# Kernel optimization log

Measured on AMD Instinct MI355X. Metric: run time of the kernel, lower is better.

The kernel has to match this reference:

```python
import jax, jax.numpy as jnp
import numpy as np

B, N, D = 8, 4096, 6          # clouds, points per cloud, coordinate dim
K = 64                        # max_num_neighbors in radius query
NS1, NS2 = 2048, 512          # fps ratios 0.5 and 0.25
R1, R2 = 0.2, 0.4             # ball-query radii
DIMS = {1: [6, 64, 64, 128], 2: [134, 128, 128, 256], 3: [262, 256, 512, 1024], 4: [1024, 512, 512]}


def setup_inputs():
    key = jax.random.key(0)
    k0, k1, k2 = jax.random.split(key, 3)
    inp = {}
    inp['synapse_cordi'] = jax.random.normal(k0, (B * N, D), jnp.float32)
    inp['batch_index'] = jnp.repeat(jnp.arange(B, dtype=jnp.int32), N)
    inp['weight'] = jax.random.uniform(k1, (B * N,), jnp.float32)
    k = k2
    for i, dims in DIMS.items():
        for j in range(len(dims) - 1):
            k, kw = jax.random.split(k)
            inp[f'w{i}_{j}'] = jax.random.normal(kw, (dims[j], dims[j + 1]), jnp.float32) * (1.0 / float(np.sqrt(dims[j])))
            inp[f'b{i}_{j}'] = jnp.zeros((dims[j + 1],), jnp.float32)
    return inp


def _mlp(x, params):
    # PyG MLP, plain_last=True; batch-norm at default (eval, running stats) is identity
    n = len(params)
    for i, (W, b) in enumerate(params):
        x = x @ W + b
        if i < n - 1:
            x = jax.nn.relu(x)
    return x


def _fps(pos, n_s):
    # farthest point sampling on one cloud [N, D] -> [n_s] indices (deterministic start at 0)
    d0 = jnp.sum((pos - pos[0]) ** 2, axis=-1)
    def step(mind, _):
        nxt = jnp.argmax(mind)
        mind = jnp.minimum(mind, jnp.sum((pos - pos[nxt]) ** 2, axis=-1))
        return mind, nxt
    _, idxs = jax.lax.scan(step, d0, None, length=n_s - 1)
    return jnp.concatenate([jnp.zeros((1,), idxs.dtype), idxs])


def _ball(pos, pos_q, r):
    # radius query: up to K nearest points within r for each query; [n_q,K] idx + validity mask
    d2 = jnp.sum((pos_q[:, None, :] - pos[None, :, :]) ** 2, axis=-1)  # [n_q, N]
    neg = jnp.where(d2 <= r * r, -d2, -jnp.inf)
    vals, nbr = jax.lax.top_k(neg, K)
    return nbr, vals > -jnp.inf


def _sa(x, pos, params, n_s, r):
    # Weight_Sample_Module: fps -> radius -> PointNetConv (gather, MLP, masked max-scatter)
    idx = jax.vmap(lambda p: _fps(p, n_s))(pos)                     # [B, n_s]
    pos_q = jnp.take_along_axis(pos, idx[..., None], axis=1)        # [B, n_s, D]
    nbr, valid = jax.vmap(lambda p, q: _ball(p, q, r))(pos, pos_q)  # [B, n_s, K]
    gather = lambda a: jax.vmap(lambda t, i: t[i])(a, nbr)          # [B, n_s, K, C]
    rel = gather(pos) - pos_q[:, :, None, :]
    feat = rel if x is None else jnp.concatenate([gather(x), rel], axis=-1)
    h = _mlp(feat, params)                                          # [B, n_s, K, C_out]
    h = jnp.where(valid[..., None], h, -jnp.inf)
    return jnp.max(h, axis=2), pos_q                                # max aggregation


def reference(synapse_cordi, batch_index, weight,
              w1_0, b1_0, w1_1, b1_1, w1_2, b1_2,
              w2_0, b2_0, w2_1, b2_1, w2_2, b2_2,
              w3_0, b3_0, w3_1, b3_1, w3_2, b3_2,
              w4_0, b4_0, w4_1, b4_1):
    pos = synapse_cordi.reshape(B, N, D)  # uniform clouds; batch_index = repeat(arange(B), N)
    p1 = [(w1_0, b1_0), (w1_1, b1_1), (w1_2, b1_2)]
    p2 = [(w2_0, b2_0), (w2_1, b2_1), (w2_2, b2_2)]
    p3 = [(w3_0, b3_0), (w3_1, b3_1), (w3_2, b3_2)]
    p4 = [(w4_0, b4_0), (w4_1, b4_1)]
    x1, pos1 = _sa(None, pos, p1, NS1, R1)   # [B, 2048, 128]
    x2, pos2 = _sa(x1, pos1, p2, NS2, R2)    # [B, 512, 256]
    h = _mlp(jnp.concatenate([x2, pos2], axis=-1), p3)  # [B, 512, 1024]
    g = jnp.max(h, axis=1)                   # global max pool -> [B, 1024]
    return _mlp(g, p4)                       # [B, 512]
```

## Files before the change

### kernel.cpp

```cpp
#include <hip/hip_runtime.h>
#include <math.h>

#define B_ 8
#define N_ 4096
#define D_ 6
#define K_ 64
#define NS1_ 2048
#define NS2_ 512

typedef float v2f __attribute__((ext_vector_type(2)));


__device__ __forceinline__ float dist2_rn(const float* __restrict__ a, const float* __restrict__ q) {
    float s = 0.f;
#pragma unroll
    for (int d = 0; d < 6; ++d) {
        float diff = __fsub_rn(a[d], q[d]);
        s = __fadd_rn(s, __fmul_rn(diff, diff));
    }
    return s;
}

__device__ __forceinline__ unsigned mapf(float x) {
    unsigned u = __float_as_uint(x);
    return (u & 0x80000000u) ? ~u : (u | 0x80000000u);
}
__device__ __forceinline__ float unmapf(unsigned u) {
    return __uint_as_float((u & 0x80000000u) ? (u & 0x7FFFFFFFu) : ~u);
}

template <int CTRL>
__device__ __forceinline__ double dppd(double k) {
    int lo = __double2loint(k), hi = __double2hiint(k);
    int nlo = __builtin_amdgcn_update_dpp(lo, lo, CTRL, 0xF, 0xF, false);
    int nhi = __builtin_amdgcn_update_dpp(hi, hi, CTRL, 0xF, 0xF, false);
    return __hiloint2double(nhi, nlo);
}


__device__ __forceinline__ void wait_flag(unsigned* f, int t) {
    if (t == 0) {
        while (__hip_atomic_load(f, __ATOMIC_RELAXED, __HIP_MEMORY_SCOPE_AGENT) == 0u)
            __builtin_amdgcn_s_sleep(32);
        __builtin_amdgcn_fence(__ATOMIC_ACQUIRE, "agent");
    }
    __syncthreads();
}


template <int NP, int NS>
__device__ __forceinline__ void fps_core(float* __restrict__ spos, int* __restrict__ sidx,
                                         double* __restrict__ part, int t) {
#pragma clang fp contract(off)
    constexpr int NT = 256;
    constexpr int P = NP / NT;
    constexpr int HP = P / 2;
    int lane = t & 63, w = t >> 6;

    v2f px2[HP][6];
#pragma unroll
    for (int j = 0; j < HP; ++j)
#pragma unroll
        for (int d = 0; d < 6; ++d) {
            px2[j][d].x = spos[(t + NT * (2 * j)) * 6 + d];
            px2[j][d].y = spos[(t + NT * (2 * j + 1)) * 6 + d];
        }

    float cx[6];
#pragma unroll
    for (int d = 0; d < 6; ++d) cx[d] = spos[d];

    v2f mind2[HP];
    float runv = -1.f;
    int runj = 0;
#pragma unroll
    for (int j = 0; j < HP; ++j) {
        v2f d2 = {0.f, 0.f};
#pragma unroll
        for (int d = 0; d < 6; ++d) {
            v2f df = px2[j][d] - cx[d];
            d2 = d2 + df * df;
        }
        mind2[j] = d2;
        if (d2.x > runv) { runv = d2.x; runj = t + NT * (2 * j); }
        if (d2.y > runv) { runv = d2.y; runj = t + NT * (2 * j + 1); }
    }

    for (int s = 1; s < NS; ++s) {
        double key = __hiloint2double((int)__float_as_uint(runv), (int)(unsigned)(~runj));
        key = fmax(key, dppd<0x111>(key));
        key = fmax(key, dppd<0x112>(key));
        key = fmax(key, dppd<0x114>(key));
        key = fmax(key, dppd<0x118>(key));
        key = fmax(key, dppd<0x142>(key));
        key = fmax(key, dppd<0x143>(key));
        if (lane == 63) part[(s & 1) * 4 + w] = key;
        __syncthreads();
        double kk = part[(s & 1) * 4 + (lane & 3)];
        kk = fmax(kk, dppd<0x111>(kk));
        kk = fmax(kk, dppd<0x112>(kk));
        int nx = ~__builtin_amdgcn_readlane(__double2loint(kk), 3);
        if (t == 0) sidx[s] = nx;

        const float2* sv2 = (const float2*)spos;
        float2 ca = sv2[nx * 3], cb = sv2[nx * 3 + 1], cc = sv2[nx * 3 + 2];
        cx[0] = ca.x; cx[1] = ca.y; cx[2] = cb.x; cx[3] = cb.y; cx[4] = cc.x; cx[5] = cc.y;

        runv = -1.f;
        runj = 0;
#pragma unroll
        for (int j = 0; j < HP; ++j) {
            v2f d2 = {0.f, 0.f};
#pragma unroll
            for (int d = 0; d < 6; ++d) {
                v2f df = px2[j][d] - cx[d];
                d2 = d2 + df * df;
            }
            float mx = fminf(mind2[j].x, d2.x);
            float my = fminf(mind2[j].y, d2.y);
            mind2[j].x = mx;
            mind2[j].y = my;
            if (mx > runv) { runv = mx; runj = t + NT * (2 * j); }
            if (my > runv) { runv = my; runj = t + NT * (2 * j + 1); }
        }
    }
}


template <int NPTS, int S>
__device__ __forceinline__ int ball_scan(const float* __restrict__ sp,
                                         const float* __restrict__ posq,
                                         float r2, int qid, int tid,
                                         float* __restrict__ sd, unsigned short* __restrict__ si) {
    float q[6];
#pragma unroll
    for (int d = 0; d < 6; ++d) q[d] = posq[(size_t)qid * 6 + d];

    int n = 0;
    float thr = INFINITY;
#pragma unroll 4
    for (int j = 0; j < NPTS; ++j) {
        float d2 = dist2_rn(sp + j * 6, q);
        if (d2 <= r2 && (n < K_ || d2 < thr)) {
            int i = (n < K_) ? n : (K_ - 1);
            if (n < K_) ++n;
            while (i > 0 && sd[(i - 1) * S + tid] > d2) {
                sd[i * S + tid] = sd[(i - 1) * S + tid];
                si[i * S + tid] = si[(i - 1) * S + tid];
                --i;
            }
            sd[i * S + tid] = d2;
            si[i * S + tid] = (unsigned short)j;
            if (n == K_) thr = sd[(K_ - 1) * S + tid];
        }
    }
    return n;
}


__global__ __launch_bounds__(256, 1) void stage12_kernel(
        const float* __restrict__ pos, float* __restrict__ pos1, float* __restrict__ pos2,
        float* __restrict__ x1, int* __restrict__ nbr2, int* __restrict__ cnt2,
        unsigned* __restrict__ g, unsigned* flags,
        const float* __restrict__ W1_0, const float* __restrict__ B1_0,
        const float* __restrict__ W1_1, const float* __restrict__ B1_1,
        const float* __restrict__ W1_2, const float* __restrict__ B1_2,
        float r2_1, float r2_2) {
    __shared__ union Smem {
        struct { float spos[N_ * 6]; int sidx[NS1_]; double part[8]; } fps;
        struct { float spos[N_ * 6]; float sd[K_ * 128]; unsigned short si[K_ * 128];
                 unsigned short scnt[128]; } p1;
        struct { float spos1[NS1_ * 6]; float sd2[K_ * 64]; unsigned short si2[K_ * 64]; } b2;
    } sm;
    int t = threadIdx.x;
    int lane = t & 63, w = t >> 6;

    if (blockIdx.x < 8) {
        int b = blockIdx.x;
        float* spos = sm.fps.spos;
        int* sidx = sm.fps.sidx;
        double* part = sm.fps.part;

        {
            const float4* src = (const float4*)(pos + (size_t)b * N_ * 6);
            float4* dst = (float4*)spos;
            for (int e = t; e < N_ * 6 / 4; e += 256) dst[e] = src[e];
        }
        if (t == 0) sidx[0] = 0;
        __syncthreads();

        fps_core<N_, NS1_>(spos, sidx, part, t);
        __syncthreads();

        float smp[NS1_ / 256][6];
#pragma unroll
        for (int i = 0; i < NS1_ / 256; ++i) {
            int s = t + 256 * i;
            int ix = sidx[s];
#pragma unroll
            for (int d = 0; d < 6; ++d) smp[i][d] = spos[ix * 6 + d];
        }
#pragma unroll
        for (int i = 0; i < NS1_ / 256; ++i) {
            int s = t + 256 * i;
#pragma unroll
            for (int d = 0; d < 6; ++d) pos1[((size_t)b * NS1_ + s) * 6 + d] = smp[i][d];
        }
        __syncthreads();
        if (t == 0) {
            __threadfence();
            __hip_atomic_store(&flags[b], 1u, __ATOMIC_RELEASE, __HIP_MEMORY_SCOPE_AGENT);
        }

#pragma unroll
        for (int i = 0; i < NS1_ / 256; ++i) {
            int s = t + 256 * i;
#pragma unroll
            for (int d = 0; d < 6; ++d) spos[s * 6 + d] = smp[i][d];
        }
        for (int e = t; e < 1024; e += 256) g[b * 1024 + e] = 0u;
        if (t == 0) sidx[0] = 0;
        __syncthreads();

        fps_core<NS1_, NS2_>(spos, sidx, part, t);
        __syncthreads();

        for (int s = t; s < NS2_; s += 256) {
            int ix = sidx[s];
#pragma unroll
            for (int d = 0; d < 6; ++d) pos2[((size_t)b * NS2_ + s) * 6 + d] = spos[ix * 6 + d];
        }
        __syncthreads();
        if (t == 0) {
            __threadfence();
            __hip_atomic_store(&flags[8 + b], 1u, __ATOMIC_RELEASE, __HIP_MEMORY_SCOPE_AGENT);
        }
    } else if (blockIdx.x < 8 + 128) {
        int blk = blockIdx.x - 8;
        int b = blk >> 4;
        {
            const float4* src = (const float4*)(pos + (size_t)b * N_ * 6);
            float4* dst = (float4*)sm.p1.spos;
            for (int e = t; e < N_ * 6 / 4; e += 256) dst[e] = src[e];
        }
        __syncthreads();
        wait_flag(&flags[b], t);

        int qbase1 = b * NS1_ + (blk & 15) * 128;
        if (t < 128) {
            int n = ball_scan<N_, 128>(sm.p1.spos, pos1, r2_1, qbase1 + t, t, sm.p1.sd, sm.p1.si);
            sm.p1.scnt[t] = (unsigned short)n;
        }
        __syncthreads();

        for (int qq = 0; qq < 32; ++qq) {
            int lq = w * 32 + qq;
            int qid = qbase1 + lq;
            float q[6];
#pragma unroll
            for (int d = 0; d < 6; ++d) q[d] = pos1[(size_t)qid * 6 + d];
            int c = sm.p1.scnt[lq];
            float m0 = -INFINITY, m1 = -INFINITY;
            for (int n = 0; n < c; ++n) {
                int j = sm.p1.si[n * 128 + lq];
                float rel[6];
#pragma unroll
                for (int d = 0; d < 6; ++d) rel[d] = sm.p1.spos[j * 6 + d] - q[d];
                float a = B1_0[lane];
#pragma unroll
                for (int d = 0; d < 6; ++d) a = fmaf(W1_0[d * 64 + lane], rel[d], a);
                float h1 = fmaxf(a, 0.f);
                float a2 = B1_1[lane];
                for (int k = 0; k < 64; ++k) {
                    float v = __shfl(h1, k, 64);
                    a2 = fmaf(W1_1[k * 64 + lane], v, a2);
                }
                float h2 = fmaxf(a2, 0.f);
                float o0 = B1_2[lane], o1 = B1_2[64 + lane];
                for (int k = 0; k < 64; ++k) {
                    float v = __shfl(h2, k, 64);
                    o0 = fmaf(W1_2[k * 128 + lane], v, o0);
                    o1 = fmaf(W1_2[k * 128 + 64 + lane], v, o1);
                }
                m0 = fmaxf(m0, o0);
                m1 = fmaxf(m1, o1);
            }
            x1[(size_t)qid * 128 + lane] = m0;
            x1[(size_t)qid * 128 + 64 + lane] = m1;
        }
    } else {
        int blk = blockIdx.x - 136;
        int b = blk >> 3;
        wait_flag(&flags[b], t);
        {
            const float4* src = (const float4*)(pos1 + (size_t)b * NS1_ * 6);
            float4* dst = (float4*)sm.b2.spos1;
            for (int e = t; e < NS1_ * 6 / 4; e += 256) dst[e] = src[e];
        }
        __syncthreads();
        wait_flag(&flags[8 + b], t);
        if (t < 64) {
            int qid = blk * 64 + t;
            int n = ball_scan<NS1_, 64>(sm.b2.spos1, pos2, r2_2, qid, t, sm.b2.sd2, sm.b2.si2);
            cnt2[qid] = n;
            for (int i = 0; i < n; ++i) nbr2[(size_t)qid * K_ + i] = (int)sm.b2.si2[i * 64 + t];
        }
    }
}


__global__ __launch_bounds__(256, 1) void sa2_mlp3_kernel(
        const float* __restrict__ pos1, const float* __restrict__ pos2,
        const int* __restrict__ nbr, const int* __restrict__ cnt,
        const float* __restrict__ x1,
        const float* __restrict__ W1, const float* __restrict__ B1,
        const float* __restrict__ W2, const float* __restrict__ B2,
        const float* __restrict__ W3, const float* __restrict__ B3,
        const float* __restrict__ M0, const float* __restrict__ MB0,
        const float* __restrict__ M1, const float* __restrict__ MB1,
        const float* __restrict__ M2, const float* __restrict__ MB2,
        unsigned* __restrict__ g) {
    __shared__ float sx2[16 * 256];
    int lane = threadIdx.x & 63;
    int w = threadIdx.x >> 6;
    int qbase = blockIdx.x * 16;
    int b = qbase >> 9;

    for (int qq = 0; qq < 4; ++qq) {
        int lq = w * 4 + qq;
        int qid = qbase + lq;
        float q[6];
#pragma unroll
        for (int d = 0; d < 6; ++d) q[d] = pos2[(size_t)qid * 6 + d];
        int c = cnt[qid];
        float m0 = -INFINITY, m1 = -INFINITY, m2 = -INFINITY, m3 = -INFINITY;
        for (int n = 0; n < c; ++n) {
            int j = nbr[(size_t)qid * K_ + n];
            size_t row = (size_t)b * NS1_ + j;
            const float* xs = x1 + row * 128;
            float rel[6];
#pragma unroll
            for (int d = 0; d < 6; ++d) rel[d] = pos1[row * 6 + d] - q[d];
            float a0e = B1[lane], a0o = 0.f, a1e = B1[64 + lane], a1o = 0.f;
            for (int k = 0; k < 128; k += 2) {
                float v0 = xs[k], v1 = xs[k + 1];
                a0e = fmaf(W1[k * 128 + lane], v0, a0e);
                a1e = fmaf(W1[k * 128 + 64 + lane], v0, a1e);
                a0o = fmaf(W1[(k + 1) * 128 + lane], v1, a0o);
                a1o = fmaf(W1[(k + 1) * 128 + 64 + lane], v1, a1o);
            }
            float a0 = a0e + a0o, a1 = a1e + a1o;
#pragma unroll
            for (int d = 0; d < 6; ++d) {
                float v = rel[d];
                a0 = fmaf(W1[(128 + d) * 128 + lane], v, a0);
                a1 = fmaf(W1[(128 + d) * 128 + 64 + lane], v, a1);
            }
            float h1a = fmaxf(a0, 0.f), h1b = fmaxf(a1, 0.f);
            float c0 = B2[lane], c1 = B2[64 + lane];
            for (int k = 0; k < 64; ++k) {
                float v = __shfl(h1a, k, 64);
                c0 = fmaf(W2[k * 128 + lane], v, c0);
                c1 = fmaf(W2[k * 128 + 64 + lane], v, c1);
            }
            for (int k = 0; k < 64; ++k) {
                float v = __shfl(h1b, k, 64);
                c0 = fmaf(W2[(64 + k) * 128 + lane], v, c0);
                c1 = fmaf(W2[(64 + k) * 128 + 64 + lane], v, c1);
            }
            float h2a = fmaxf(c0, 0.f), h2b = fmaxf(c1, 0.f);
            float e0 = B3[lane], e1 = B3[64 + lane], e2 = B3[128 + lane], e3 = B3[192 + lane];
            for (int k = 0; k < 64; ++k) {
                float v = __shfl(h2a, k, 64);
                e0 = fmaf(W3[k * 256 + lane], v, e0);
                e1 = fmaf(W3[k * 256 + 64 + lane], v, e1);
                e2 = fmaf(W3[k * 256 + 128 + lane], v, e2);
                e3 = fmaf(W3[k * 256 + 192 + lane], v, e3);
            }
            for (int k = 0; k < 64; ++k) {
                float v = __shfl(h2b, k, 64);
                e0 = fmaf(W3[(64 + k) * 256 + lane], v, e0);
                e1 = fmaf(W3[(64 + k) * 256 + 64 + lane], v, e1);
                e2 = fmaf(W3[(64 + k) * 256 + 128 + lane], v, e2);
                e3 = fmaf(W3[(64 + k) * 256 + 192 + lane], v, e3);
            }
            m0 = fmaxf(m0, e0);
            m1 = fmaxf(m1, e1);
            m2 = fmaxf(m2, e2);
            m3 = fmaxf(m3, e3);
        }
        sx2[lq * 256 + lane] = m0;
        sx2[lq * 256 + 64 + lane] = m1;
        sx2[lq * 256 + 128 + lane] = m2;
        sx2[lq * 256 + 192 + lane] = m3;
    }
    __syncthreads();

    int lq0 = w * 4;
    int qid0 = qbase + lq0;

    float xr[4][4];
#pragma unroll
    for (int q = 0; q < 4; ++q)
#pragma unroll
        for (int j = 0; j < 4; ++j) xr[q][j] = sx2[(lq0 + q) * 256 + j * 64 + lane];

    float a[4][4];
    {
        float4 bv = *(const float4*)&MB0[lane * 4];
#pragma unroll
        for (int q = 0; q < 4; ++q) { a[q][0] = bv.x; a[q][1] = bv.y; a[q][2] = bv.z; a[q][3] = bv.w; }
    }
#pragma unroll
    for (int j = 0; j < 4; ++j) {
        for (int k2 = 0; k2 < 64; ++k2) {
            int k = j * 64 + k2;
            float4 wv = *(const float4*)&M0[(size_t)k * 256 + lane * 4];
#pragma unroll
            for (int q = 0; q < 4; ++q) {
                float v = __shfl(xr[q][j], k2, 64);
                a[q][0] = fmaf(wv.x, v, a[q][0]);
                a[q][1] = fmaf(wv.y, v, a[q][1]);
                a[q][2] = fmaf(wv.z, v, a[q][2]);
                a[q][3] = fmaf(wv.w, v, a[q][3]);
            }
        }
    }
#pragma unroll
    for (int d = 0; d < 6; ++d) {
        float4 wv = *(const float4*)&M0[(size_t)(256 + d) * 256 + lane * 4];
#pragma unroll
        for (int q = 0; q < 4; ++q) {
            float v = pos2[(size_t)(qid0 + q) * 6 + d];
            a[q][0] = fmaf(wv.x, v, a[q][0]);
            a[q][1] = fmaf(wv.y, v, a[q][1]);
            a[q][2] = fmaf(wv.z, v, a[q][2]);
            a[q][3] = fmaf(wv.w, v, a[q][3]);
        }
    }
    float h1[4][4];
#pragma unroll
    for (int q = 0; q < 4; ++q)
#pragma unroll
        for (int u = 0; u < 4; ++u) h1[q][u] = fmaxf(a[q][u], 0.f);

    float c[4][8];
    {
        float4 b0 = *(const float4*)&MB1[lane * 8];
        float4 b1 = *(const float4*)&MB1[lane * 8 + 4];
#pragma unroll
        for (int q = 0; q < 4; ++q) {
            c[q][0] = b0.x; c[q][1] = b0.y; c[q][2] = b0.z; c[q][3] = b0.w;
            c[q][4] = b1.x; c[q][5] = b1.y; c[q][6] = b1.z; c[q][7] = b1.w;
        }
    }
    for (int l = 0; l < 64; ++l) {
#pragma unroll
        for (int r = 0; r < 4; ++r) {
            int k = l * 4 + r;
            float4 w0 = *(const float4*)&M1[(size_t)k * 512 + lane * 8];
            float4 w1 = *(const float4*)&M1[(size_t)k * 512 + lane * 8 + 4];
#pragma unroll
            for (int q = 0; q < 4; ++q) {
                float v = __shfl(h1[q][r], l, 64);
                c[q][0] = fmaf(w0.x, v, c[q][0]);
                c[q][1] = fmaf(w0.y, v, c[q][1]);
                c[q][2] = fmaf(w0.z, v, c[q][2]);
                c[q][3] = fmaf(w0.w, v, c[q][3]);
                c[q][4] = fmaf(w1.x, v, c[q][4]);
                c[q][5] = fmaf(w1.y, v, c[q][5]);
                c[q][6] = fmaf(w1.z, v, c[q][6]);
                c[q][7] = fmaf(w1.w, v, c[q][7]);
            }
        }
    }
    float h2[4][8];
#pragma unroll
    for (int q = 0; q < 4; ++q)
#pragma unroll
        for (int u = 0; u < 8; ++u) h2[q][u] = fmaxf(c[q][u], 0.f);

    float e[4][16];
#pragma unroll
    for (int jj = 0; jj < 4; ++jj) {
        float4 bv = *(const float4*)&MB2[lane * 16 + jj * 4];
#pragma unroll
        for (int q = 0; q < 4; ++q) {
            e[q][jj * 4 + 0] = bv.x; e[q][jj * 4 + 1] = bv.y;
            e[q][jj * 4 + 2] = bv.z; e[q][jj * 4 + 3] = bv.w;
        }
    }
    for (int l = 0; l < 64; ++l) {
#pragma unroll
        for (int r = 0; r < 8; ++r) {
            int k = l * 8 + r;
            const float* wp = &M2[(size_t)k * 1024 + lane * 16];
            float4 w0 = *(const float4*)&wp[0];
            float4 w1 = *(const float4*)&wp[4];
            float4 w2 = *(const float4*)&wp[8];
            float4 w3 = *(const float4*)&wp[12];
#pragma unroll
            for (int q = 0; q < 4; ++q) {
                float v = __shfl(h2[q][r], l, 64);
                e[q][0]  = fmaf(w0.x, v, e[q][0]);
                e[q][1]  = fmaf(w0.y, v, e[q][1]);
                e[q][2]  = fmaf(w0.z, v, e[q][2]);
                e[q][3]  = fmaf(w0.w, v, e[q][3]);
                e[q][4]  = fmaf(w1.x, v, e[q][4]);
                e[q][5]  = fmaf(w1.y, v, e[q][5]);
                e[q][6]  = fmaf(w1.z, v, e[q][6]);
                e[q][7]  = fmaf(w1.w, v, e[q][7]);
                e[q][8]  = fmaf(w2.x, v, e[q][8]);
                e[q][9]  = fmaf(w2.y, v, e[q][9]);
                e[q][10] = fmaf(w2.z, v, e[q][10]);
                e[q][11] = fmaf(w2.w, v, e[q][11]);
                e[q][12] = fmaf(w3.x, v, e[q][12]);
                e[q][13] = fmaf(w3.y, v, e[q][13]);
                e[q][14] = fmaf(w3.z, v, e[q][14]);
                e[q][15] = fmaf(w3.w, v, e[q][15]);
            }
        }
    }
#pragma unroll
    for (int u = 0; u < 16; ++u) {
        float m = fmaxf(fmaxf(e[0][u], e[1][u]), fmaxf(e[2][u], e[3][u]));
        atomicMax(&g[b * 1024 + lane * 16 + u], mapf(m));
    }
}


__global__ __launch_bounds__(512) void mlp4_kernel(const unsigned* __restrict__ g,
                                                   const float* __restrict__ W0, const float* __restrict__ B0,
                                                   const float* __restrict__ W1, const float* __restrict__ B1,
                                                   float* __restrict__ out) {
    int b = blockIdx.x;
    int c = threadIdx.x;
    __shared__ float h[512];
    float a0 = B0[c], a1 = 0.f, a2 = 0.f, a3 = 0.f;
    for (int k = 0; k < 1024; k += 4) {
        float v0 = unmapf(g[b * 1024 + k]);
        float v1 = unmapf(g[b * 1024 + k + 1]);
        float v2 = unmapf(g[b * 1024 + k + 2]);
        float v3 = unmapf(g[b * 1024 + k + 3]);
        a0 = fmaf(v0, W0[k * 512 + c], a0);
        a1 = fmaf(v1, W0[(k + 1) * 512 + c], a1);
        a2 = fmaf(v2, W0[(k + 2) * 512 + c], a2);
        a3 = fmaf(v3, W0[(k + 3) * 512 + c], a3);
    }
    h[c] = fmaxf((a0 + a1) + (a2 + a3), 0.f);
    __syncthreads();
    float o0 = B1[c], o1 = 0.f, o2 = 0.f, o3 = 0.f;
    for (int k = 0; k < 512; k += 4) {
        o0 = fmaf(h[k], W1[k * 512 + c], o0);
        o1 = fmaf(h[k + 1], W1[(k + 1) * 512 + c], o1);
        o2 = fmaf(h[k + 2], W1[(k + 2) * 512 + c], o2);
        o3 = fmaf(h[k + 3], W1[(k + 3) * 512 + c], o3);
    }
    out[(size_t)b * 512 + c] = (o0 + o1) + (o2 + o3);
}


extern "C" void kernel_launch(void* const* d_in, const int* in_sizes, int n_in,
                              void* d_out, int out_size, void* d_ws, size_t ws_size,
                              hipStream_t stream) {
    const float* pos = (const float*)d_in[0];
    const float* w1_0 = (const float*)d_in[3];
    const float* b1_0 = (const float*)d_in[4];
    const float* w1_1 = (const float*)d_in[5];
    const float* b1_1 = (const float*)d_in[6];
    const float* w1_2 = (const float*)d_in[7];
    const float* b1_2 = (const float*)d_in[8];
    const float* w2_0 = (const float*)d_in[9];
    const float* b2_0 = (const float*)d_in[10];
    const float* w2_1 = (const float*)d_in[11];
    const float* b2_1 = (const float*)d_in[12];
    const float* w2_2 = (const float*)d_in[13];
    const float* b2_2 = (const float*)d_in[14];
    const float* w3_0 = (const float*)d_in[15];
    const float* b3_0 = (const float*)d_in[16];
    const float* w3_1 = (const float*)d_in[17];
    const float* b3_1 = (const float*)d_in[18];
    const float* w3_2 = (const float*)d_in[19];
    const float* b3_2 = (const float*)d_in[20];
    const float* w4_0 = (const float*)d_in[21];
    const float* b4_0 = (const float*)d_in[22];
    const float* w4_1 = (const float*)d_in[23];
    const float* b4_1 = (const float*)d_in[24];
    float* out = (float*)d_out;

    char* ws = (char*)d_ws;
    size_t off = 0;
    float* pos1 = (float*)(ws + off);    off += (size_t)B_ * NS1_ * 6 * 4;
    float* pos2 = (float*)(ws + off);    off += (size_t)B_ * NS2_ * 6 * 4;
    float* x1 = (float*)(ws + off);      off += (size_t)B_ * NS1_ * 128 * 4;
    int* nbr2 = (int*)(ws + off);        off += (size_t)B_ * NS2_ * K_ * 4;
    int* cnt2 = (int*)(ws + off);        off += (size_t)B_ * NS2_ * 4;
    unsigned* g = (unsigned*)(ws + off); off += (size_t)B_ * 1024 * 4;
    unsigned* flags = (unsigned*)(ws + off); off += 16 * 4;

    const float r2_1 = (float)(0.2 * 0.2);
    const float r2_2 = (float)(0.4 * 0.4);

    hipMemsetAsync(flags, 0, 16 * 4, stream);

    stage12_kernel<<<200, 256, 0, stream>>>(pos, pos1, pos2, x1, nbr2, cnt2, g, flags,
                                            w1_0, b1_0, w1_1, b1_1, w1_2, b1_2,
                                            r2_1, r2_2);
    sa2_mlp3_kernel<<<(B_ * NS2_) / 16, 256, 0, stream>>>(pos1, pos2, nbr2, cnt2, x1,
                                                          w2_0, b2_0, w2_1, b2_1, w2_2, b2_2,
                                                          w3_0, b3_0, w3_1, b3_1, w3_2, b3_2, g);
    mlp4_kernel<<<B_, 512, 0, stream>>>(g, w4_0, b4_0, w4_1, b4_1, out);
}
```

Baseline: 2.498 ms.

## Fuse SA2, MLP3 and MLP4 into one persistent kernel with per-cloud flag counters

Merges the three launches into a single 200-block persistent kernel. The 128 SA1 blocks go on to run SA2 and MLP3 for their own cloud once counter flags report that SA1, FPS2 and ball-query results are ready. The FPS blocks finish with the final MLP4 once all 16 tail blocks for their cloud signal completion. Weights are pre-read into cache while blocks wait. This removes launch gaps and lets clouds proceed independently, but runs SA2/MLP3 on only 128 blocks instead of 256 and relies on all blocks being co-resident for the spin-waits.

After: 3.790 ms. +51.7%, slower.

```diff
diff --git a/kernel.cpp b/kernel.cpp
--- a/kernel.cpp
+++ b/kernel.cpp
@@ -45,6 +45,23 @@
         __builtin_amdgcn_fence(__ATOMIC_ACQUIRE, "agent");
     }
     __syncthreads();
+}
+
+__device__ __forceinline__ void wait_count(unsigned* f, unsigned tgt, int t) {
+    if (t == 0) {
+        while (__hip_atomic_load(f, __ATOMIC_RELAXED, __HIP_MEMORY_SCOPE_AGENT) < tgt)
+            __builtin_amdgcn_s_sleep(8);
+        __builtin_amdgcn_fence(__ATOMIC_ACQUIRE, "agent");
+    }
+    __syncthreads();
+}
+
+__device__ __forceinline__ void release_add(unsigned* f, int t) {
+    __syncthreads();
+    if (t == 0) {
+        __threadfence();
+        __hip_atomic_fetch_add(f, 1u, __ATOMIC_RELEASE, __HIP_MEMORY_SCOPE_AGENT);
+    }
 }
 
 
@@ -158,13 +175,275 @@
 }
 
 
-__global__ __launch_bounds__(256, 1) void stage12_kernel(
+__device__ __forceinline__ void sa2_one(int qid, int lane,
+        const float* __restrict__ pos1, const float* __restrict__ posq,
+        const int* __restrict__ nbr, const int* __restrict__ cnt,
+        const float* __restrict__ x1,
+        const float* __restrict__ W1, const float* __restrict__ B1,
+        const float* __restrict__ W2, const float* __restrict__ B2,
+        const float* __restrict__ W3, const float* __restrict__ B3,
+        float* __restrict__ out) {
+    int b = qid / NS2_;
+    float q[6];
+#pragma unroll
+    for (int d = 0; d < 6; ++d) q[d] = posq[(size_t)qid * 6 + d];
+    int c = cnt[qid];
+    float m0 = -INFINITY, m1 = -INFINITY, m2 = -INFINITY, m3 = -INFINITY;
+
+    for (int n = 0; n < c; ++n) {
+        int j = nbr[(size_t)qid * K_ + n];
+        size_t row = (size_t)b * NS1_ + j;
+        const float* xs = x1 + row * 128;
+        float rel[6];
+#pragma unroll
+        for (int d = 0; d < 6; ++d) rel[d] = pos1[row * 6 + d] - q[d];
+        float a0e = B1[lane], a0o = 0.f, a1e = B1[64 + lane], a1o = 0.f;
+        for (int k = 0; k < 128; k += 2) {
+            float v0 = xs[k], v1 = xs[k + 1];
+            a0e = fmaf(W1[k * 128 + lane], v0, a0e);
+            a1e = fmaf(W1[k * 128 + 64 + lane], v0, a1e);
+            a0o = fmaf(W1[(k + 1) * 128 + lane], v1, a0o);
+            a1o = fmaf(W1[(k + 1) * 128 + 64 + lane], v1, a1o);
+        }
+        float a0 = a0e + a0o, a1 = a1e + a1o;
+#pragma unroll
+        for (int d = 0; d < 6; ++d) {
+            float v = rel[d];
+            a0 = fmaf(W1[(128 + d) * 128 + lane], v, a0);
+            a1 = fmaf(W1[(128 + d) * 128 + 64 + lane], v, a1);
+        }
+        float h1a = fmaxf(a0, 0.f), h1b = fmaxf(a1, 0.f);
+        float c0 = B2[lane], c1 = B2[64 + lane];
+        for (int k = 0; k < 64; ++k) {
+            float v = __shfl(h1a, k, 64);
+            c0 = fmaf(W2[k * 128 + lane], v, c0);
+            c1 = fmaf(W2[k * 128 + 64 + lane], v, c1);
+        }
+        for (int k = 0; k < 64; ++k) {
+            float v = __shfl(h1b, k, 64);
+            c0 = fmaf(W2[(64 + k) * 128 + lane], v, c0);
+            c1 = fmaf(W2[(64 + k) * 128 + 64 + lane], v, c1);
+        }
+        float h2a = fmaxf(c0, 0.f), h2b = fmaxf(c1, 0.f);
+        float e0 = B3[lane], e1 = B3[64 + lane], e2 = B3[128 + lane], e3 = B3[192 + lane];
+        for (int k = 0; k < 64; ++k) {
+            float v = __shfl(h2a, k, 64);
+            e0 = fmaf(W3[k * 256 + lane], v, e0);
+            e1 = fmaf(W3[k * 256 + 64 + lane], v, e1);
+            e2 = fmaf(W3[k * 256 + 128 + lane], v, e2);
+            e3 = fmaf(W3[k * 256 + 192 + lane], v, e3);
+        }
+        for (int k = 0; k < 64; ++k) {
+            float v = __shfl(h2b, k, 64);
+            e0 = fmaf(W3[(64 + k) * 256 + lane], v, e0);
+            e1 = fmaf(W3[(64 + k) * 256 + 64 + lane], v, e1);
+            e2 = fmaf(W3[(64 + k) * 256 + 128 + lane], v, e2);
+            e3 = fmaf(W3[(64 + k) * 256 + 192 + lane], v, e3);
+        }
+        m0 = fmaxf(m0, e0);
+        m1 = fmaxf(m1, e1);
+        m2 = fmaxf(m2, e2);
+        m3 = fmaxf(m3, e3);
+    }
+    out[(size_t)qid * 256 + lane] = m0;
+    out[(size_t)qid * 256 + 64 + lane] = m1;
+    out[(size_t)qid * 256 + 128 + lane] = m2;
+    out[(size_t)qid * 256 + 192 + lane] = m3;
+}
+
+
+__device__ __forceinline__ void mlp3_wave(int qid0, int lane,
+        const float* __restrict__ x2, const float* __restrict__ pos2,
+        const float* __restrict__ M0, const float* __restrict__ MB0,
+        const float* __restrict__ M1, const float* __restrict__ MB1,
+        const float* __restrict__ M2, const float* __restrict__ MB2,
+        unsigned* __restrict__ g) {
+    int b = qid0 >> 9;
+
+    float xr[4][4];
+#pragma unroll
+    for (int q = 0; q < 4; ++q)
+#pragma unroll
+        for (int j = 0; j < 4; ++j) xr[q][j] = x2[(size_t)(qid0 + q) * 256 + j * 64 + lane];
+
+    float a[4][4];
+    {
+        float4 bv = *(const float4*)&MB0[lane * 4];
+#pragma unroll
+        for (int q = 0; q < 4; ++q) { a[q][0] = bv.x; a[q][1] = bv.y; a[q][2] = bv.z; a[q][3] = bv.w; }
+    }
+#pragma unroll
+    for (int j = 0; j < 4; ++j) {
+        for (int k2 = 0; k2 < 64; ++k2) {
+            int k = j * 64 + k2;
+            float4 wv = *(const float4*)&M0[(size_t)k * 256 + lane * 4];
+#pragma unroll
+            for (int q = 0; q < 4; ++q) {
+                float v = __shfl(xr[q][j], k2, 64);
+                a[q][0] = fmaf(wv.x, v, a[q][0]);
+                a[q][1] = fmaf(wv.y, v, a[q][1]);
+                a[q][2] = fmaf(wv.z, v, a[q][2]);
+                a[q][3] = fmaf(wv.w, v, a[q][3]);
+            }
+        }
+    }
+#pragma unroll
+    for (int d = 0; d < 6; ++d) {
+        float4 wv = *(const float4*)&M0[(size_t)(256 + d) * 256 + lane * 4];
+#pragma unroll
+        for (int q = 0; q < 4; ++q) {
+            float v = pos2[(size_t)(qid0 + q) * 6 + d];
+            a[q][0] = fmaf(wv.x, v, a[q][0]);
+            a[q][1] = fmaf(wv.y, v, a[q][1]);
+            a[q][2] = fmaf(wv.z, v, a[q][2]);
+            a[q][3] = fmaf(wv.w, v, a[q][3]);
+        }
+    }
+    float h1[4][4];
+#pragma unroll
+    for (int q = 0; q < 4; ++q)
+#pragma unroll
+        for (int u = 0; u < 4; ++u) h1[q][u] = fmaxf(a[q][u], 0.f);
+
+    float c[4][8];
+    {
+        float4 b0 = *(const float4*)&MB1[lane * 8];
+        float4 b1 = *(const float4*)&MB1[lane * 8 + 4];
+#pragma unroll
+        for (int q = 0; q < 4; ++q) {
+            c[q][0] = b0.x; c[q][1] = b0.y; c[q][2] = b0.z; c[q][3] = b0.w;
+            c[q][4] = b1.x; c[q][5] = b1.y; c[q][6] = b1.z; c[q][7] = b1.w;
+        }
+    }
+    for (int l = 0; l < 64; ++l) {
+#pragma unroll
+        for (int r = 0; r < 4; ++r) {
+            int k = l * 4 + r;
+            float4 w0 = *(const float4*)&M1[(size_t)k * 512 + lane * 8];
+            float4 w1 = *(const float4*)&M1[(size_t)k * 512 + lane * 8 + 4];
+#pragma unroll
+            for (int q = 0; q < 4; ++q) {
+                float v = __shfl(h1[q][r], l, 64);
+                c[q][0] = fmaf(w0.x, v, c[q][0]);
+                c[q][1] = fmaf(w0.y, v, c[q][1]);
+                c[q][2] = fmaf(w0.z, v, c[q][2]);
+                c[q][3] = fmaf(w0.w, v, c[q][3]);
+                c[q][4] = fmaf(w1.x, v, c[q][4]);
+                c[q][5] = fmaf(w1.y, v, c[q][5]);
+                c[q][6] = fmaf(w1.z, v, c[q][6]);
+                c[q][7] = fmaf(w1.w, v, c[q][7]);
+            }
+        }
+    }
+    float h2[4][8];
+#pragma unroll
+    for (int q = 0; q < 4; ++q)
+#pragma unroll
+        for (int u = 0; u < 8; ++u) h2[q][u] = fmaxf(c[q][u], 0.f);
+
+    float e[4][16];
+#pragma unroll
+    for (int jj = 0; jj < 4; ++jj) {
+        float4 bv = *(const float4*)&MB2[lane * 16 + jj * 4];
+#pragma unroll
+        for (int q = 0; q < 4; ++q) {
+            e[q][jj * 4 + 0] = bv.x; e[q][jj * 4 + 1] = bv.y;
+            e[q][jj * 4 + 2] = bv.z; e[q][jj * 4 + 3] = bv.w;
+        }
+    }
+    for (int l = 0; l < 64; ++l) {
+#pragma unroll
+        for (int r = 0; r < 8; ++r) {
+            int k = l * 8 + r;
+            const float* wp = &M2[(size_t)k * 1024 + lane * 16];
+            float4 w0 = *(const float4*)&wp[0];
+            float4 w1 = *(const float4*)&wp[4];
+            float4 w2 = *(const float4*)&wp[8];
+            float4 w3 = *(const float4*)&wp[12];
+#pragma unroll
+            for (int q = 0; q < 4; ++q) {
+                float v = __shfl(h2[q][r], l, 64);
+                e[q][0]  = fmaf(w0.x, v, e[q][0]);
+                e[q][1]  = fmaf(w0.y, v, e[q][1]);
+                e[q][2]  = fmaf(w0.z, v, e[q][2]);
+                e[q][3]  = fmaf(w0.w, v, e[q][3]);
+                e[q][4]  = fmaf(w1.x, v, e[q][4]);
+                e[q][5]  = fmaf(w1.y, v, e[q][5]);
+                e[q][6]  = fmaf(w1.z, v, e[q][6]);
+                e[q][7]  = fmaf(w1.w, v, e[q][7]);
+                e[q][8]  = fmaf(w2.x, v, e[q][8]);
+                e[q][9]  = fmaf(w2.y, v, e[q][9]);
+                e[q][10] = fmaf(w2.z, v, e[q][10]);
+                e[q][11] = fmaf(w2.w, v, e[q][11]);
+                e[q][12] = fmaf(w3.x, v, e[q][12]);
+                e[q][13] = fmaf(w3.y, v, e[q][13]);
+                e[q][14] = fmaf(w3.z, v, e[q][14]);
+                e[q][15] = fmaf(w3.w, v, e[q][15]);
+            }
+        }
+    }
+#pragma unroll
+    for (int u = 0; u < 16; ++u) {
+        float m = fmaxf(fmaxf(e[0][u], e[1][u]), fmaxf(e[2][u], e[3][u]));
+        atomicMax(&g[b * 1024 + lane * 16 + u], mapf(m));
+    }
+}
+
+
+__device__ __attribute__((noinline)) void tail_sa2_mlp3(int b, int sub, int t,
+        const float* pos1, const float* pos2,
+        const int* nbr2, const int* cnt2, const float* x1, float* x2,
+        const float* W2_0, const float* B2_0, const float* W2_1, const float* B2_1,
+        const float* W2_2, const float* B2_2,
+        const float* M0, const float* MB0, const float* M1, const float* MB1,
+        const float* M2, const float* MB2, unsigned* g) {
+    int lane = t & 63, w = t >> 6;
+    int qbase = b * NS2_ + sub * 32;
+    for (int i = 0; i < 8; ++i)
+        sa2_one(qbase + w * 8 + i, lane, pos1, pos2, nbr2, cnt2, x1,
+                W2_0, B2_0, W2_1, B2_1, W2_2, B2_2, x2);
+    __syncthreads();
+    for (int p = 0; p < 2; ++p)
+        mlp3_wave(qbase + p * 16 + w * 4, lane, x2, pos2, M0, MB0, M1, MB1, M2, MB2, g);
+}
+
+__device__ __attribute__((noinline)) void tail_mlp4(int b, int t,
+        const unsigned* g, const float* W0, const float* B0,
+        const float* W1, const float* B1, float* out) {
+    __shared__ float h[512];
+    for (int ch = t; ch < 512; ch += 256) {
+        float a = B0[ch];
+        for (int k = 0; k < 1024; ++k) {
+            float v = unmapf(g[b * 1024 + k]);
+            a = fmaf(v, W0[k * 512 + ch], a);
+        }
+        h[ch] = fmaxf(a, 0.f);
+    }
+    __syncthreads();
+    for (int ch = t; ch < 512; ch += 256) {
+        float o = B1[ch];
+        for (int k = 0; k < 512; ++k) o = fmaf(h[k], W1[k * 512 + ch], o);
+        out[(size_t)b * 512 + ch] = o;
+    }
+}
+
+
+__global__ __launch_bounds__(256, 1) void stage_all_kernel(
         const float* __restrict__ pos, float* __restrict__ pos1, float* __restrict__ pos2,
-        float* __restrict__ x1, int* __restrict__ nbr2, int* __restrict__ cnt2,
-        unsigned* __restrict__ g, unsigned* flags,
+        float* __restrict__ x1, float* __restrict__ x2,
+        int* __restrict__ nbr2, int* __restrict__ cnt2,
+        unsigned* __restrict__ g, unsigned* flags, float* __restrict__ out,
         const float* __restrict__ W1_0, const float* __restrict__ B1_0,
         const float* __restrict__ W1_1, const float* __restrict__ B1_1,
         const float* __restrict__ W1_2, const float* __restrict__ B1_2,
+        const float* __restrict__ W2_0, const float* __restrict__ B2_0,
+        const float* __restrict__ W2_1, const float* __restrict__ B2_1,
+        const float* __restrict__ W2_2, const float* __restrict__ B2_2,
+        const float* __restrict__ M0, const float* __restrict__ MB0,
+        const float* __restrict__ M1, const float* __restrict__ MB1,
+        const float* __restrict__ M2, const float* __restrict__ MB2,
+        const float* __restrict__ W4_0, const float* __restrict__ B4_0,
+        const float* __restrict__ W4_1, const float* __restrict__ B4_1,
         float r2_1, float r2_2) {
     __shared__ union Smem {
         struct { float spos[N_ * 6]; int sidx[NS1_]; double part[8]; } fps;
@@ -235,9 +514,18 @@
             __threadfence();
             __hip_atomic_store(&flags[8 + b], 1u, __ATOMIC_RELEASE, __HIP_MEMORY_SCOPE_AGENT);
         }
+
+        {
+            float acc = 0.f;
+            for (int e = t; e < 1024 * 512; e += 256) acc += W4_0[e];
+            for (int e = t; e < 512 * 512; e += 256) acc += W4_1[e];
+            asm volatile("" :: "v"(acc));
+        }
+        wait_count(&flags[32 + b], 16u, t);
+        tail_mlp4(b, t, g, W4_0, B4_0, W4_1, B4_1, out);
     } else if (blockIdx.x < 8 + 128) {
         int blk = blockIdx.x - 8;
-        int b = blk >> 4;
+        int b = blk >> 4, sub = blk & 15;
         {
             const float4* src = (const float4*)(pos + (size_t)b * N_ * 6);
             float4* dst = (float4*)sm.p1.spos;
@@ -246,7 +534,7 @@
         __syncthreads();
         wait_flag(&flags[b], t);
 
-        int qbase1 = b * NS1_ + (blk & 15) * 128;
+        int qbase1 = b * NS1_ + sub * 128;
         if (t < 128) {
             int n = ball_scan<N_, 128>(sm.p1.spos, pos1, r2_1, qbase1 + t, t, sm.p1.sd, sm.p1.si);
             sm.p1.scnt[t] = (unsigned short)n;
@@ -288,6 +576,27 @@
             x1[(size_t)qid * 128 + lane] = m0;
             x1[(size_t)qid * 128 + 64 + lane] = m1;
         }
+        release_add(&flags[16 + b], t);
+
+        {
+            float acc = 0.f;
+            for (int e = t; e < 134 * 128; e += 256) acc += W2_0[e];
+            for (int e = t; e < 128 * 128; e += 256) acc += W2_1[e];
+            for (int e = t; e < 128 * 256; e += 256) acc += W2_2[e];
+            for (int e = t; e < 262 * 256; e += 256) acc += M0[e];
+            for (int e = t; e < 256 * 512; e += 256) acc += M1[e];
+            for (int e = t; e < 512 * 1024; e += 256) acc += M2[e];
+            asm volatile("" :: "v"(acc));
+        }
+
+        wait_flag(&flags[8 + b], t);
+        wait_count(&flags[24 + b], 8u, t);
+        wait_count(&flags[16 + b], 16u, t);
+
+        tail_sa2_mlp3(b, sub, t, pos1, pos2, nbr2, cnt2, x1, x2,
+                      W2_0, B2_0, W2_1, B2_1, W2_2, B2_2,
+                      M0, MB0, M1, MB1, M2, MB2, g);
+        release_add(&flags[32 + b], t);
     } else {
         int blk = blockIdx.x - 136;
         int b = blk >> 3;
@@ -305,258 +614,8 @@
             cnt2[qid] = n;
             for (int i = 0; i < n; ++i) nbr2[(size_t)qid * K_ + i] = (int)sm.b2.si2[i * 64 + t];
         }
-    }
-}
-
-
-__global__ __launch_bounds__(256, 1) void sa2_mlp3_kernel(
-        const float* __restrict__ pos1, const float* __restrict__ pos2,
-        const int* __restrict__ nbr, const int* __restrict__ cnt,
-        const float* __restrict__ x1,
-        const float* __restrict__ W1, const float* __restrict__ B1,
-        const float* __restrict__ W2, const float* __restrict__ B2,
-        const float* __restrict__ W3, const float* __restrict__ B3,
-        const float* __restrict__ M0, const float* __restrict__ MB0,
-        const float* __restrict__ M1, const float* __restrict__ MB1,
-        const float* __restrict__ M2, const float* __restrict__ MB2,
-        unsigned* __restrict__ g) {
-    __shared__ float sx2[16 * 256];
-    int lane = threadIdx.x & 63;
-    int w = threadIdx.x >> 6;
-    int qbase = blockIdx.x * 16;
-    int b = qbase >> 9;
-
-    for (int qq = 0; qq < 4; ++qq) {
-        int lq = w * 4 + qq;
-        int qid = qbase + lq;
-        float q[6];
-#pragma unroll
-        for (int d = 0; d < 6; ++d) q[d] = pos2[(size_t)qid * 6 + d];
-        int c = cnt[qid];
-        float m0 = -INFINITY, m1 = -INFINITY, m2 = -INFINITY, m3 = -INFINITY;
-        for (int n = 0; n < c; ++n) {
-            int j = nbr[(size_t)qid * K_ + n];
-            size_t row = (size_t)b * NS1_ + j;
-            const float* xs = x1 + row * 128;
-            float rel[6];
-#pragma unroll
-            for (int d = 0; d < 6; ++d) rel[d] = pos1[row * 6 + d] - q[d];
-            float a0e = B1[lane], a0o = 0.f, a1e = B1[64 + lane], a1o = 0.f;
-            for (int k = 0; k < 128; k += 2) {
-                float v0 = xs[k], v1 = xs[k + 1];
-                a0e = fmaf(W1[k * 128 + lane], v0, a0e);
-                a1e = fmaf(W1[k * 128 + 64 + lane], v0, a1e);
-                a0o = fmaf(W1[(k + 1) * 128 + lane], v1, a0o);
-                a1o = fmaf(W1[(k + 1) * 128 + 64 + lane], v1, a1o);
-            }
-            float a0 = a0e + a0o, a1 = a1e + a1o;
-#pragma unroll
-            for (int d = 0; d < 6; ++d) {
-                float v = rel[d];
-                a0 = fmaf(W1[(128 + d) * 128 + lane], v, a0);
-                a1 = fmaf(W1[(128 + d) * 128 + 64 + lane], v, a1);
-            }
-            float h1a = fmaxf(a0, 0.f), h1b = fmaxf(a1, 0.f);
-            float c0 = B2[lane], c1 = B2[64 + lane];
-            for (int k = 0; k < 64; ++k) {
-                float v = __shfl(h1a, k, 64);
-                c0 = fmaf(W2[k * 128 + lane], v, c0);
-                c1 = fmaf(W2[k * 128 + 64 + lane], v, c1);
-            }
-            for (int k = 0; k < 64; ++k) {
-                float v = __shfl(h1b, k, 64);
-                c0 = fmaf(W2[(64 + k) * 128 + lane], v, c0);
-                c1 = fmaf(W2[(64 + k) * 128 + 64 + lane], v, c1);
-            }
-            float h2a = fmaxf(c0, 0.f), h2b = fmaxf(c1, 0.f);
-            float e0 = B3[lane], e1 = B3[64 + lane], e2 = B3[128 + lane], e3 = B3[192 + lane];
-            for (int k = 0; k < 64; ++k) {
-                float v = __shfl(h2a, k, 64);
-                e0 = fmaf(W3[k * 256 + lane], v, e0);
-                e1 = fmaf(W3[k * 256 + 64 + lane], v, e1);
-                e2 = fmaf(W3[k * 256 + 128 + lane], v, e2);
-                e3 = fmaf(W3[k * 256 + 192 + lane], v, e3);
-            }
-            for (int k = 0; k < 64; ++k) {
-                float v = __shfl(h2b, k, 64);
-                e0 = fmaf(W3[(64 + k) * 256 + lane], v, e0);
-                e1 = fmaf(W3[(64 + k) * 256 + 64 + lane], v, e1);
-                e2 = fmaf(W3[(64 + k) * 256 + 128 + lane], v, e2);
-                e3 = fmaf(W3[(64 + k) * 256 + 192 + lane], v, e3);
-            }
-            m0 = fmaxf(m0, e0);
-            m1 = fmaxf(m1, e1);
-            m2 = fmaxf(m2, e2);
-            m3 = fmaxf(m3, e3);
-        }
-        sx2[lq * 256 + lane] = m0;
-        sx2[lq * 256 + 64 + lane] = m1;
-        sx2[lq * 256 + 128 + lane] = m2;
-        sx2[lq * 256 + 192 + lane] = m3;
-    }
-    __syncthreads();
-
-    int lq0 = w * 4;
-    int qid0 = qbase + lq0;
-
-    float xr[4][4];
-#pragma unroll
-    for (int q = 0; q < 4; ++q)
-#pragma unroll
-        for (int j = 0; j < 4; ++j) xr[q][j] = sx2[(lq0 + q) * 256 + j * 64 + lane];
-
-    float a[4][4];
-    {
-        float4 bv = *(const float4*)&MB0[lane * 4];
-#pragma unroll
-        for (int q = 0; q < 4; ++q) { a[q][0] = bv.x; a[q][1] = bv.y; a[q][2] = bv.z; a[q][3] = bv.w; }
-    }
-#pragma unroll
-    for (int j = 0; j < 4; ++j) {
-        for (int k2 = 0; k2 < 64; ++k2) {
-            int k = j * 64 + k2;
-            float4 wv = *(const float4*)&M0[(size_t)k * 256 + lane * 4];
-#pragma unroll
-            for (int q = 0; q < 4; ++q) {
-                float v = __shfl(xr[q][j], k2, 64);
-                a[q][0] = fmaf(wv.x, v, a[q][0]);
-                a[q][1] = fmaf(wv.y, v, a[q][1]);
-                a[q][2] = fmaf(wv.z, v, a[q][2]);
-                a[q][3] = fmaf(wv.w, v, a[q][3]);
-            }
-        }
-    }
-#pragma unroll
-    for (int d = 0; d < 6; ++d) {
-        float4 wv = *(const float4*)&M0[(size_t)(256 + d) * 256 + lane * 4];
-#pragma unroll
-        for (int q = 0; q < 4; ++q) {
-            float v = pos2[(size_t)(qid0 + q) * 6 + d];
-            a[q][0] = fmaf(wv.x, v, a[q][0]);
-            a[q][1] = fmaf(wv.y, v, a[q][1]);
-            a[q][2] = fmaf(wv.z, v, a[q][2]);
-            a[q][3] = fmaf(wv.w, v, a[q][3]);
-        }
-    }
-    float h1[4][4];
-#pragma unroll
-    for (int q = 0; q < 4; ++q)
-#pragma unroll
-        for (int u = 0; u < 4; ++u) h1[q][u] = fmaxf(a[q][u], 0.f);
-
-    float c[4][8];
-    {
-        float4 b0 = *(const float4*)&MB1[lane * 8];
-        float4 b1 = *(const float4*)&MB1[lane * 8 + 4];
-#pragma unroll
-        for (int q = 0; q < 4; ++q) {
-            c[q][0] = b0.x; c[q][1] = b0.y; c[q][2] = b0.z; c[q][3] = b0.w;
-            c[q][4] = b1.x; c[q][5] = b1.y; c[q][6] = b1.z; c[q][7] = b1.w;
-        }
-    }
-    for (int l = 0; l < 64; ++l) {
-#pragma unroll
-        for (int r = 0; r < 4; ++r) {
-            int k = l * 4 + r;
-            float4 w0 = *(const float4*)&M1[(size_t)k * 512 + lane * 8];
-            float4 w1 = *(const float4*)&M1[(size_t)k * 512 + lane * 8 + 4];
-#pragma unroll
-            for (int q = 0; q < 4; ++q) {
-                float v = __shfl(h1[q][r], l, 64);
-                c[q][0] = fmaf(w0.x, v, c[q][0]);
-                c[q][1] = fmaf(w0.y, v, c[q][1]);
-                c[q][2] = fmaf(w0.z, v, c[q][2]);
-                c[q][3] = fmaf(w0.w, v, c[q][3]);
-                c[q][4] = fmaf(w1.x, v, c[q][4]);
-                c[q][5] = fmaf(w1.y, v, c[q][5]);
-                c[q][6] = fmaf(w1.z, v, c[q][6]);
-                c[q][7] = fmaf(w1.w, v, c[q][7]);
-            }
-        }
-    }
-    float h2[4][8];
-#pragma unroll
-    for (int q = 0; q < 4; ++q)
-#pragma unroll
-        for (int u = 0; u < 8; ++u) h2[q][u] = fmaxf(c[q][u], 0.f);
-
-    float e[4][16];
-#pragma unroll
-    for (int jj = 0; jj < 4; ++jj) {
-        float4 bv = *(const float4*)&MB2[lane * 16 + jj * 4];
-#pragma unroll
-        for (int q = 0; q < 4; ++q) {
-            e[q][jj * 4 + 0] = bv.x; e[q][jj * 4 + 1] = bv.y;
-            e[q][jj * 4 + 2] = bv.z; e[q][jj * 4 + 3] = bv.w;
-        }
-    }
-    for (int l = 0; l < 64; ++l) {
-#pragma unroll
-        for (int r = 0; r < 8; ++r) {
-            int k = l * 8 + r;
-            const float* wp = &M2[(size_t)k * 1024 + lane * 16];
-            float4 w0 = *(const float4*)&wp[0];
-            float4 w1 = *(const float4*)&wp[4];
-            float4 w2 = *(const float4*)&wp[8];
-            float4 w3 = *(const float4*)&wp[12];
-#pragma unroll
-            for (int q = 0; q < 4; ++q) {
-                float v = __shfl(h2[q][r], l, 64);
-                e[q][0]  = fmaf(w0.x, v, e[q][0]);
-                e[q][1]  = fmaf(w0.y, v, e[q][1]);
-                e[q][2]  = fmaf(w0.z, v, e[q][2]);
-                e[q][3]  = fmaf(w0.w, v, e[q][3]);
-                e[q][4]  = fmaf(w1.x, v, e[q][4]);
-                e[q][5]  = fmaf(w1.y, v, e[q][5]);
-                e[q][6]  = fmaf(w1.z, v, e[q][6]);
-                e[q][7]  = fmaf(w1.w, v, e[q][7]);
-                e[q][8]  = fmaf(w2.x, v, e[q][8]);
-                e[q][9]  = fmaf(w2.y, v, e[q][9]);
-                e[q][10] = fmaf(w2.z, v, e[q][10]);
-                e[q][11] = fmaf(w2.w, v, e[q][11]);
-                e[q][12] = fmaf(w3.x, v, e[q][12]);
-                e[q][13] = fmaf(w3.y, v, e[q][13]);
-                e[q][14] = fmaf(w3.z, v, e[q][14]);
-                e[q][15] = fmaf(w3.w, v, e[q][15]);
-            }
-        }
-    }
-#pragma unroll
-    for (int u = 0; u < 16; ++u) {
-        float m = fmaxf(fmaxf(e[0][u], e[1][u]), fmaxf(e[2][u], e[3][u]));
-        atomicMax(&g[b * 1024 + lane * 16 + u], mapf(m));
-    }
-}
-
-
-__global__ __launch_bounds__(512) void mlp4_kernel(const unsigned* __restrict__ g,
-                                                   const float* __restrict__ W0, const float* __restrict__ B0,
-                                                   const float* __restrict__ W1, const float* __restrict__ B1,
-                                                   float* __restrict__ out) {
-    int b = blockIdx.x;
-    int c = threadIdx.x;
-    __shared__ float h[512];
-    float a0 = B0[c], a1 = 0.f, a2 = 0.f, a3 = 0.f;
-    for (int k = 0; k < 1024; k += 4) {
-        float v0 = unmapf(g[b * 1024 + k]);
-        float v1 = unmapf(g[b * 1024 + k + 1]);
-        float v2 = unmapf(g[b * 1024 + k + 2]);
-        float v3 = unmapf(g[b * 1024 + k + 3]);
-        a0 = fmaf(v0, W0[k * 512 + c], a0);
-        a1 = fmaf(v1, W0[(k + 1) * 512 + c], a1);
-        a2 = fmaf(v2, W0[(k + 2) * 512 + c], a2);
-        a3 = fmaf(v3, W0[(k + 3) * 512 + c], a3);
-    }
-    h[c] = fmaxf((a0 + a1) + (a2 + a3), 0.f);
-    __syncthreads();
-    float o0 = B1[c], o1 = 0.f, o2 = 0.f, o3 = 0.f;
-    for (int k = 0; k < 512; k += 4) {
-        o0 = fmaf(h[k], W1[k * 512 + c], o0);
-        o1 = fmaf(h[k + 1], W1[(k + 1) * 512 + c], o1);
-        o2 = fmaf(h[k + 2], W1[(k + 2) * 512 + c], o2);
-        o3 = fmaf(h[k + 3], W1[(k + 3) * 512 + c], o3);
-    }
-    out[(size_t)b * 512 + c] = (o0 + o1) + (o2 + o3);
+        release_add(&flags[24 + b], t);
+    }
 }
 
 
@@ -593,21 +652,21 @@
     float* pos1 = (float*)(ws + off);    off += (size_t)B_ * NS1_ * 6 * 4;
     float* pos2 = (float*)(ws + off);    off += (size_t)B_ * NS2_ * 6 * 4;
     float* x1 = (float*)(ws + off);      off += (size_t)B_ * NS1_ * 128 * 4;
+    float* x2 = (float*)(ws + off);      off += (size_t)B_ * NS2_ * 256 * 4;
     int* nbr2 = (int*)(ws + off);        off += (size_t)B_ * NS2_ * K_ * 4;
     int* cnt2 = (int*)(ws + off);        off += (size_t)B_ * NS2_ * 4;
     unsigned* g = (unsigned*)(ws + off); off += (size_t)B_ * 1024 * 4;
-    unsigned* flags = (unsigned*)(ws + off); off += 16 * 4;
+    unsigned* flags = (unsigned*)(ws + off); off += 64 * 4;
 
     const float r2_1 = (float)(0.2 * 0.2);
     const float r2_2 = (float)(0.4 * 0.4);
 
-    hipMemsetAsync(flags, 0, 16 * 4, stream);
-
-    stage12_kernel<<<200, 256, 0, stream>>>(pos, pos1, pos2, x1, nbr2, cnt2, g, flags,
-                                            w1_0, b1_0, w1_1, b1_1, w1_2, b1_2,
-                                            r2_1, r2_2);
-    sa2_mlp3_kernel<<<(B_ * NS2_) / 16, 256, 0, stream>>>(pos1, pos2, nbr2, cnt2, x1,
-                                                          w2_0, b2_0, w2_1, b2_1, w2_2, b2_2,
-                                                          w3_0, b3_0, w3_1, b3_1, w3_2, b3_2, g);
-    mlp4_kernel<<<B_, 512, 0, stream>>>(g, w4_0, b4_0, w4_1, b4_1, out);
-}
+    hipMemsetAsync(flags, 0, 64 * 4, stream);
+
+    stage_all_kernel<<<200, 256, 0, stream>>>(pos, pos1, pos2, x1, x2, nbr2, cnt2, g, flags, out,
+                                              w1_0, b1_0, w1_1, b1_1, w1_2, b1_2,
+                                              w2_0, b2_0, w2_1, b2_1, w2_2, b2_2,
+                                              w3_0, b3_0, w3_1, b3_1, w3_2, b3_2,
+                                              w4_0, b4_0, w4_1, b4_1,
+                                              r2_1, r2_2);
+}
```
